# Kernel tuning notes

Hardware: AMD Instinct MI355X
Metric: run time of the kernel (lower is better)

Reference implementation:

```python
import jax, jax.numpy as jnp
import numpy as np

B, N, DIM = 4, 4096, 512
HEADS, DHEAD, CHUNK = 4, 128, 64
MAX_LR = 1.0
EPS = 1e-6


def rmsnorm(x):
    return x * jax.lax.rsqrt(jnp.mean(x * x, axis=-1, keepdims=True) + EPS)


def mem_mlp(params, x):
    # MemoryMLP depth=2: x @ W1 -> silu -> @ W2 (no biases)
    W1, W2 = params
    return jax.nn.silu(x @ W1) @ W2


def assoc_scan(gates, x):
    # linear recurrence y_i = g_i * y_{i-1} + x_i along axis=1 (chunks)
    def op(a, b):
        ga, xa = a
        gb, xb = b
        return (ga * gb, gb * xa + xb)
    _, y = jax.lax.associative_scan(op, (gates, x), axis=1)
    return y


def setup_inputs() -> dict:
    key = jax.random.key(0)
    ks = jax.random.split(key, 12)
    di = HEADS * DHEAD
    nrm = lambda k, shp, sc: jax.random.normal(k, shp, jnp.float32) * sc
    return {
        'seq': nrm(ks[0], (B, N, DIM), 1.0),
        'g_store': jnp.ones((DIM,), jnp.float32),
        'g_retrieve': jnp.ones((DIM,), jnp.float32),
        'W_q': nrm(ks[1], (DIM, di), DIM ** -0.5),
        'W_kv': nrm(ks[2], (DIM, 2 * di), DIM ** -0.5),
        'W_step': nrm(ks[3], (DIM, HEADS), DIM ** -0.5),
        'W_mom': nrm(ks[4], (DIM, HEADS), DIM ** -0.5),
        'W_decay': nrm(ks[5], (DIM, HEADS), DIM ** -0.5),
        'W_gate': nrm(ks[6], (DIM, HEADS), DIM ** -0.5),
        'gamma_mh': jnp.zeros((HEADS, 1, DHEAD), jnp.float32),
        'W_o': nrm(ks[7], (di, DIM), di ** -0.5),
        'M_W1': nrm(ks[8], (DHEAD, DHEAD), DHEAD ** -0.5),
        'M_W2': nrm(ks[9], (DHEAD, DHEAD), DHEAD ** -0.5),
    }


def reference(seq, g_store, g_retrieve, W_q, W_kv, W_step, W_mom, W_decay,
              W_gate, gamma_mh, W_o, M_W1, M_W2):
    b, n, dim = seq.shape
    h, d, c = HEADS, DHEAD, CHUNK
    nc = n // c
    bh = b * h

    # ---------------- store path ----------------
    s = rmsnorm(seq) * g_store                                   # (b,n,dim)
    lr = jax.nn.sigmoid(s @ W_step) * MAX_LR                     # (b,n,h)
    lr_c = lr.transpose(0, 2, 1).reshape(bh, nc, c)              # (bh,nc,c)
    chunked = s.reshape(b, nc, c, dim).mean(2)                   # (b,nc,dim)
    decay = jax.nn.sigmoid(chunked @ W_decay).transpose(0, 2, 1).reshape(bh, nc)
    mom = jax.nn.sigmoid(chunked @ W_mom).transpose(0, 2, 1).reshape(bh, nc)

    kv = s @ W_kv                                                # (b,n,2*h*d)
    k, v = jnp.split(kv, 2, axis=-1)
    to_chunks = lambda t: t.reshape(b, n, h, d).transpose(0, 2, 1, 3).reshape(bh, nc, c, d)
    k, v = to_chunks(k), to_chunks(v)

    # per-chunk gradient at the initial memory weights (vmap(grad))
    def chunk_loss(params, kc, lrc, vc):
        pred = mem_mlp(params, kc)                               # (c,d)
        loss = jnp.mean((pred - vc) ** 2, axis=-1)               # (c,)
        return jnp.sum(loss * lrc)

    gfn = jax.vmap(jax.vmap(jax.grad(chunk_loss),
                            in_axes=((None, None), 0, 0, 0)),
                   in_axes=((None, None), 0, 0, 0))
    g1, g2 = gfn((M_W1, M_W2), k, lr_c, v)                       # (bh,nc,d,d)
    s1, s2 = -g1, -g2                                            # surprises

    # momentum assoc scan: m_i = mom_i * m_{i-1} + s_i
    momg = mom[:, :, None, None]
    m1 = assoc_scan(momg, s1)
    m2 = assoc_scan(momg, s2)

    # decay-gated weight recurrence with prev = initial weights:
    # W_i = (1 - decay_i) * W_{i-1} + m_i,  W_0 = init
    def scan_with_init(gates, x, w0):
        g = jnp.concatenate([jnp.ones_like(gates[:, :1]), gates], axis=1)
        x0 = jnp.broadcast_to(w0, (bh, 1) + w0.shape)
        return assoc_scan(g, jnp.concatenate([x0, x], axis=1))   # (bh,nc+1,d,d)

    dg = (1.0 - decay)[:, :, None, None]
    u1 = scan_with_init(dg, m1, M_W1)
    u2 = scan_with_init(dg, m2, M_W2)
    # retrieval for chunk i uses weights after chunk i-1 (paper semantics)
    w1c, w2c = u1[:, :-1], u2[:, :-1]                            # (bh,nc,d,d)

    # ---------------- retrieve path ----------------
    r = rmsnorm(seq) * g_retrieve
    q = to_chunks(r @ W_q)                                       # (bh,nc,c,d)
    pred = jax.vmap(jax.vmap(lambda w1, w2, qc: mem_mlp((w1, w2), qc)))(w1c, w2c, q)
    out = pred.reshape(b, h, n, d)
    out = rmsnorm(out) * (gamma_mh + 1.0)                        # multihead rmsnorm
    gate = jax.nn.sigmoid(r @ W_gate)                            # (b,n,h)
    out = out * gate.transpose(0, 2, 1)[..., None]               # retrieve gate
    out = out.transpose(0, 2, 1, 3).reshape(b, n, h * d)         # merge heads
    return out @ W_o                                             # combine heads
```

## Files before the change

### kernel.cpp

```cpp
#include <hip/hip_runtime.h>

typedef unsigned short u16;
typedef unsigned int u32;
typedef __attribute__((ext_vector_type(8))) short s16x8;
typedef __attribute__((ext_vector_type(4))) float f32x4;

#define DEV __device__ __forceinline__
#define MFMA16(a,b,c) __builtin_amdgcn_mfma_f32_16x16x32_bf16(a,b,c,0,0,0)

DEV float bf2f(u16 x){ u32 u=((u32)x)<<16; float f; __builtin_memcpy(&f,&u,4); return f; }
DEV u16 f2bf(float f){ u32 u; __builtin_memcpy(&u,&f,4); u32 r=u+0x7FFFu+((u>>16)&1u); return (u16)(r>>16); }
DEV uint4 pack8(const float* f){
  uint4 v;
  v.x=(u32)f2bf(f[0])|((u32)f2bf(f[1])<<16);
  v.y=(u32)f2bf(f[2])|((u32)f2bf(f[3])<<16);
  v.z=(u32)f2bf(f[4])|((u32)f2bf(f[5])<<16);
  v.w=(u32)f2bf(f[6])|((u32)f2bf(f[7])<<16);
  return v;
}
DEV float sigm(float x){ return 1.0f/(1.0f+__expf(-x)); }


DEV void trans_tile_a(const float* src, u16* dst, int K, int Nn, int bx, int by,
                      int tid, bool act, float* ld)
{
  int n0 = bx*64, k0 = by*64;
  if (act){
    #pragma unroll
    for (int rr=0; rr<4; rr++){
      int kk = rr*16 + (tid>>4);
      int nn = (tid&15)*4;
      float4 v = *(const float4*)(src + (size_t)(k0+kk)*Nn + n0 + nn);
      ld[kk*65+nn]=v.x; ld[kk*65+nn+1]=v.y; ld[kk*65+nn+2]=v.z; ld[kk*65+nn+3]=v.w;
    }
  }
  __syncthreads();
  if (act){
    int nn2 = tid>>2, kb = (tid&3)*16;
    float o[16];
    #pragma unroll
    for (int j=0;j<16;j++) o[j] = ld[(kb+j)*65+nn2];
    u16* dp = dst + (size_t)(n0+nn2)*K + k0 + kb;
    *(uint4*)dp     = pack8(&o[0]);
    *(uint4*)(dp+8) = pack8(&o[8]);
  }
}

__global__ __launch_bounds__(512) void k_front(const float* __restrict__ seq,
    const float* __restrict__ gs, const float* __restrict__ gr,
    const float* __restrict__ Wstep, const float* __restrict__ Wgate,
    const float* __restrict__ Wdec, const float* __restrict__ Wmom,
    const float* __restrict__ Wkv, const float* __restrict__ Wq,
    const float* __restrict__ Wo, const float* __restrict__ MW1,
    const float* __restrict__ MW2,
    u16* __restrict__ s, u16* __restrict__ r,
    float* __restrict__ lr, float* __restrict__ gate,
    float* __restrict__ momv, float* __restrict__ dgv,
    u16* __restrict__ Wkvt, u16* __restrict__ Wqt, u16* __restrict__ Wot,
    u16* __restrict__ W1t, u16* __restrict__ W2t, u16* __restrict__ W2s)
{
  __shared__ float smem[8192];
  const int blk = blockIdx.x;
  const int tid = threadIdx.x;

  if (blk >= 256){
    int l = blk - 256;
    bool act = tid < 256;
    int t2 = tid & 255;
    if (l < 128)      trans_tile_a(Wkv, Wkvt, 512, 1024, l&15, l>>4, t2, act, smem);
    else if (l < 192){ int m = l-128; trans_tile_a(Wq, Wqt, 512, 512, m&7, m>>3, t2, act, smem); }
    else if (l < 256){ int m = l-192; trans_tile_a(Wo, Wot, 512, 512, m&7, m>>3, t2, act, smem); }
    else if (l < 260){ int m = l-256; trans_tile_a(MW1, W1t, 128, 128, m&1, m>>1, t2, act, smem); }
    else if (l < 264){ int m = l-260; trans_tile_a(MW2, W2t, 128, 128, m&1, m>>1, t2, act, smem); }
    else {
      __syncthreads();
      if (act){
        int e = ((l-264)*256 + t2)*8;
        float f[8];
        *(float4*)&f[0] = *(const float4*)(MW2+e);
        *(float4*)&f[4] = *(const float4*)(MW2+e+4);
        *(uint4*)(W2s+e) = pack8(f);
      }
    }
    return;
  }

  float* pchunk = smem;
  float* red    = smem + 4096;
  const int b = blk >> 6, ci = blk & 63;
  const int wv = tid >> 6, lane = tid & 63;
  const size_t rowbase = (size_t)b*4096 + (size_t)ci*64;

  float psum[8] = {0,0,0,0,0,0,0,0};
  #pragma unroll 1
  for (int tt=0; tt<8; tt++){
    int t = wv*8 + tt;
    const float* row = seq + (rowbase + t)*512;
    float x[8];
    *(float4*)&x[0] = *(const float4*)(row + lane*8);
    *(float4*)&x[4] = *(const float4*)(row + lane*8 + 4);
    float ss = 0.f;
    #pragma unroll
    for (int j=0;j<8;j++) ss += x[j]*x[j];
    #pragma unroll
    for (int o=32;o>=1;o>>=1) ss += __shfl_xor(ss, o, 64);
    float inv = rsqrtf(ss*(1.0f/512.0f) + 1e-6f);
    float al[4] = {0,0,0,0}, ag[4] = {0,0,0,0};
    float sv8[8], rv8[8];
    #pragma unroll
    for (int j=0;j<8;j++){
      int d = lane*8 + j;
      float sn = x[j]*inv;
      float sv = sn*gs[d];
      float rv = sn*gr[d];
      sv8[j]=sv; rv8[j]=rv;
      psum[j] += sv;
      float4 wst = *(const float4*)(Wstep + d*4);
      float4 wgt = *(const float4*)(Wgate + d*4);
      al[0]+=sv*wst.x; al[1]+=sv*wst.y; al[2]+=sv*wst.z; al[3]+=sv*wst.w;
      ag[0]+=rv*wgt.x; ag[1]+=rv*wgt.y; ag[2]+=rv*wgt.z; ag[3]+=rv*wgt.w;
    }
    *(uint4*)(s + (rowbase+t)*512 + lane*8) = pack8(sv8);
    *(uint4*)(r + (rowbase+t)*512 + lane*8) = pack8(rv8);
    #pragma unroll
    for (int o=32;o>=1;o>>=1){
      #pragma unroll
      for (int h=0;h<4;h++){ al[h] += __shfl_xor(al[h], o, 64); ag[h] += __shfl_xor(ag[h], o, 64); }
    }
    if (lane == 0){
      #pragma unroll
      for (int h=0;h<4;h++){
        lr[(rowbase+t)*4 + h]   = sigm(al[h]);
        gate[(rowbase+t)*4 + h] = sigm(ag[h]);
      }
    }
  }
  #pragma unroll
  for (int j=0;j<8;j++) pchunk[wv*512 + lane*8+j] = psum[j];
  __syncthreads();
  {
    int d = tid;
    float mean = 0.f;
    #pragma unroll
    for (int w=0;w<8;w++) mean += pchunk[w*512 + d];
    mean *= (1.0f/64.0f);
    #pragma unroll
    for (int h=0;h<4;h++){
      red[h*512 + d]     = mean*Wdec[d*4+h];
      red[(4+h)*512 + d] = mean*Wmom[d*4+h];
    }
  }
  __syncthreads();
  {
    float sum = 0.f;
    #pragma unroll
    for (int j=0;j<8;j++) sum += red[wv*512 + lane*8+j];
    #pragma unroll
    for (int o=32;o>=1;o>>=1) sum += __shfl_xor(sum, o, 64);
    if (lane == 0){
      if (wv < 4) dgv[((size_t)(b*4+wv))*64 + ci]      = 1.0f - sigm(sum);
      else        momv[((size_t)(b*4+(wv-4)))*64 + ci] = sigm(sum);
    }
  }
}

template<bool OUT_BF>
DEV void gemm_body(const u16* A, const u16* Bt, void* Cv, int K, int ldc,
                   int bx, int by, u16* sA, u16* sB)
{
  const int tid = threadIdx.x;
  const int wv = tid>>6, lane = tid&63, lrow = lane&15, lk = lane>>4;
  const int wm = (wv>>1)*64, wn = (wv&1)*64;
  const int rowbase = by*128, colbase = bx*128;
  const int srow = lane>>3;
  const int scol = (lane&7)*8;
  f32x4 acc[4][4] = {};
  for (int kc = 0; kc < K; kc += 64){
    __syncthreads();
    #pragma unroll
    for (int it=0; it<4; ++it){
      int seg = it*4 + wv;
      int row = seg*8 + srow;
      __builtin_amdgcn_global_load_lds(
        (const __attribute__((address_space(1))) void*)(A + (size_t)(rowbase+row)*K + kc + scol),
        (__attribute__((address_space(3))) void*)&sA[seg*512 + lane*8], 16, 0, 0);
      __builtin_amdgcn_global_load_lds(
        (const __attribute__((address_space(1))) void*)(Bt + (size_t)(colbase+row)*K + kc + scol),
        (__attribute__((address_space(3))) void*)&sB[seg*512 + lane*8], 16, 0, 0);
    }
    __syncthreads();
    #pragma unroll
    for (int k0=0;k0<2;k0++){
      s16x8 a[4], b[4];
      #pragma unroll
      for (int m=0;m<4;m++) a[m] = *(const s16x8*)&sA[(wm+m*16+lrow)*64 + k0*32 + lk*8];
      #pragma unroll
      for (int n=0;n<4;n++) b[n] = *(const s16x8*)&sB[(wn+n*16+lrow)*64 + k0*32 + lk*8];
      #pragma unroll
      for (int m=0;m<4;m++)
        #pragma unroll
        for (int n=0;n<4;n++)
          acc[m][n] = MFMA16(a[m], b[n], acc[m][n]);
    }
  }
  #pragma unroll
  for (int m=0;m<4;m++)
    #pragma unroll
    for (int n=0;n<4;n++)
      #pragma unroll
      for (int r=0;r<4;r++){
        int row = rowbase + wm + m*16 + lk*4 + r;
        int col = colbase + wn + n*16 + lrow;
        float v = acc[m][n][r];
        if (OUT_BF) ((u16*)Cv)[(size_t)row*ldc + col] = f2bf(v);
        else        ((float*)Cv)[(size_t)row*ldc + col] = v;
      }
}

__global__ __launch_bounds__(256) void k_gemmAB(const u16* __restrict__ A1,
    const u16* __restrict__ B1, u16* __restrict__ C1,
    const u16* __restrict__ A2, const u16* __restrict__ B2, u16* __restrict__ C2)
{
  __shared__ u16 sA[128*64];
  __shared__ u16 sB[128*64];
  int bid = blockIdx.x;
  if (bid < 1024){
    int s = (bid & 7)*128 + (bid >> 3);
    gemm_body<true>(A1, B1, C1, 512, 1024, s & 7, s >> 3, sA, sB);
  } else {
    int l = bid - 1024;
    int s = (l & 7)*64 + (l >> 3);
    gemm_body<true>(A2, B2, C2, 512, 512, s & 3, s >> 2, sA, sB);
  }
}

template<bool OUT_BF>
__global__ __launch_bounds__(256) void k_gemm1(const u16* __restrict__ A,
    const u16* __restrict__ Bt, void* __restrict__ Cv, int K, int ldc, int nbx, int cpx)
{
  __shared__ u16 sA[128*64];
  __shared__ u16 sB[128*64];
  int bid = blockIdx.x;
  int s = (bid & 7)*cpx + (bid >> 3);
  gemm_body<OUT_BF>(A, Bt, Cv, K, ldc, s % nbx, s / nbx, sA, sB);
}

__global__ __launch_bounds__(256,4) void k_grad(const u16* __restrict__ kv,
    const float* __restrict__ lr, const u16* __restrict__ W1t,
    const u16* __restrict__ W2t, const u16* __restrict__ W2s,
    u16* __restrict__ s1, u16* __restrict__ s2)
{
  __shared__ u16 bufR[64*136];
  __shared__ u16 bufAt[128*68];
  __shared__ u16 bufPt[128*68];
  __shared__ float lrs[64];

  const int blk = blockIdx.x;
  const int bhi = blk >> 6, ci = blk & 63;
  const int b = bhi >> 2, hd = bhi & 3;
  const int tid = threadIdx.x;
  const int wv = tid>>6, lane = tid&63, lrow = lane&15, lk = lane>>4;
  int col[2]; col[0] = wv*32 + lrow; col[1] = wv*32 + 16 + lrow;
  const int f_hi[2] = { (lrow>>3)*128, ((16+lrow)>>3)*128 };
  const int f_lo[2] = { lrow&7, (16+lrow)&7 };
  const int fbase = wv*512;
  const size_t rowbase = (size_t)b*4096 + (size_t)ci*64;
  const u16* kvb = kv + rowbase*1024 + hd*128;

  #pragma unroll
  for (int rep=0;rep<4;rep++){
    int lin = rep*2048 + tid*8;
    int i = lin >> 7, d = lin & 127;
    *(uint4*)&bufR[i*136 + d]  = *(const uint4*)(kvb + (size_t)i*1024 + d);
    *(uint4*)&bufPt[i*136 + d] = *(const uint4*)(kvb + (size_t)i*1024 + 512 + d);
  }
  if (tid < 64) lrs[tid] = lr[(rowbase + tid)*4 + hd] * (2.0f/128.0f);
  __syncthreads();

  float spv[4][2][4];

  {
    f32x4 acc[4][2] = {};
    #pragma unroll
    for (int k0=0;k0<4;k0++){
      s16x8 w0 = *(const s16x8*)(W1t + col[0]*128 + k0*32 + lk*8);
      s16x8 w1 = *(const s16x8*)(W1t + col[1]*128 + k0*32 + lk*8);
      #pragma unroll
      for (int m=0;m<4;m++){
        s16x8 a = *(const s16x8*)&bufR[(m*16+lrow)*136 + k0*32 + lk*8];
        acc[m][0] = MFMA16(a, w0, acc[m][0]);
        acc[m][1] = MFMA16(a, w1, acc[m][1]);
      }
    }
    __syncthreads();
    #pragma unroll
    for (int m=0;m<4;m++)
      #pragma unroll
      for (int n=0;n<2;n++){
        int row0 = m*16 + lk*4;
        u16 av4[4];
        #pragma unroll
        for (int r=0;r<4;r++){
          float h = acc[m][n][r];
          float sg = sigm(h);
          av4[r] = f2bf(h*sg);
          spv[m][n][r] = sg*(1.0f + h*(1.0f - sg));
          bufR[(row0+r)*136 + col[n]] = av4[r];
        }
        *(uint2*)&bufAt[col[n]*68 + row0] = make_uint2(
          (u32)av4[0] | ((u32)av4[1]<<16), (u32)av4[2] | ((u32)av4[3]<<16));
      }
  }
  __syncthreads();

  {
    f32x4 acc[4][2] = {};
    #pragma unroll
    for (int k0=0;k0<4;k0++){
      s16x8 w0 = *(const s16x8*)(W2t + col[0]*128 + k0*32 + lk*8);
      s16x8 w1 = *(const s16x8*)(W2t + col[1]*128 + k0*32 + lk*8);
      #pragma unroll
      for (int m=0;m<4;m++){
        s16x8 a = *(const s16x8*)&bufR[(m*16+lrow)*136 + k0*32 + lk*8];
        acc[m][0] = MFMA16(a, w0, acc[m][0]);
        acc[m][1] = MFMA16(a, w1, acc[m][1]);
      }
    }
    u16 vv[4][2][4];
    #pragma unroll
    for (int m=0;m<4;m++)
      #pragma unroll
      for (int n=0;n<2;n++)
        #pragma unroll
        for (int r=0;r<4;r++)
          vv[m][n][r] = bufPt[(m*16+lk*4+r)*136 + col[n]];
    __syncthreads();
    #pragma unroll
    for (int m=0;m<4;m++)
      #pragma unroll
      for (int n=0;n<2;n++){
        int row0 = m*16 + lk*4;
        u16 dp4[4];
        #pragma unroll
        for (int r=0;r<4;r++){
          float dp = lrs[row0+r]*(acc[m][n][r] - bf2f(vv[m][n][r]));
          dp4[r] = f2bf(dp);
          bufR[(row0+r)*136 + col[n]] = dp4[r];
        }
        *(uint2*)&bufPt[col[n]*68 + row0] = make_uint2(
          (u32)dp4[0] | ((u32)dp4[1]<<16), (u32)dp4[2] | ((u32)dp4[3]<<16));
      }
  }
  __syncthreads();

  {
    f32x4 da[4][2] = {};
    #pragma unroll
    for (int k0=0;k0<4;k0++){
      s16x8 w0 = *(const s16x8*)(W2s + col[0]*128 + k0*32 + lk*8);
      s16x8 w1 = *(const s16x8*)(W2s + col[1]*128 + k0*32 + lk*8);
      #pragma unroll
      for (int m=0;m<4;m++){
        s16x8 a = *(const s16x8*)&bufR[(m*16+lrow)*136 + k0*32 + lk*8];
        da[m][0] = MFMA16(a, w0, da[m][0]);
        da[m][1] = MFMA16(a, w1, da[m][1]);
      }
    }
    __syncthreads();
    #pragma unroll
    for (int m=0;m<4;m++)
      #pragma unroll
      for (int n=0;n<2;n++){
        int row0 = m*16 + lk*4;
        u16 dh4[4];
        #pragma unroll
        for (int r=0;r<4;r++) dh4[r] = f2bf(spv[m][n][r]*da[m][n][r]);
        *(uint2*)&bufR[col[n]*68 + row0] = make_uint2(
          (u32)dh4[0] | ((u32)dh4[1]<<16), (u32)dh4[2] | ((u32)dh4[3]<<16));
      }
  }

  const size_t outbase = (size_t)blk * 16384;

  s16x8 kbf[2][2];
  #pragma unroll
  for (int n=0;n<2;n++)
    #pragma unroll
    for (int k0=0;k0<2;k0++)
      #pragma unroll
      for (int j=0;j<8;j++)
        ((u16*)&kbf[n][k0])[j] = kvb[(size_t)(k0*32 + lk*8 + j)*1024 + col[n]];
  {
    f32x4 acc[8][2] = {};
    #pragma unroll
    for (int k0=0;k0<2;k0++){
      s16x8 bf0 = *(const s16x8*)&bufAt[col[0]*68 + k0*32 + lk*8];
      s16x8 bf1 = *(const s16x8*)&bufAt[col[1]*68 + k0*32 + lk*8];
      #pragma unroll
      for (int m=0;m<8;m++){
        s16x8 a = *(const s16x8*)&bufPt[(m*16+lrow)*68 + k0*32 + lk*8];
        acc[m][0] = MFMA16(a, bf0, acc[m][0]);
        acc[m][1] = MFMA16(a, bf1, acc[m][1]);
      }
    }
    #pragma unroll
    for (int m=0;m<8;m++)
      #pragma unroll
      for (int n=0;n<2;n++)
        #pragma unroll
        for (int r=0;r<4;r++)
          s2[outbase + m*2048 + fbase + f_hi[n] + (lk*4+r)*8 + f_lo[n]] = f2bf(-acc[m][n][r]);
  }
  __syncthreads();

  {
    f32x4 acc[8][2] = {};
    #pragma unroll
    for (int k0=0;k0<2;k0++)
      #pragma unroll
      for (int m=0;m<8;m++){
        s16x8 a = *(const s16x8*)&bufR[(m*16+lrow)*68 + k0*32 + lk*8];
        acc[m][0] = MFMA16(a, kbf[0][k0], acc[m][0]);
        acc[m][1] = MFMA16(a, kbf[1][k0], acc[m][1]);
      }
    #pragma unroll
    for (int m=0;m<8;m++)
      #pragma unroll
      for (int n=0;n<2;n++)
        #pragma unroll
        for (int r=0;r<4;r++)
          s1[outbase + m*2048 + fbase + f_hi[n] + (lk*4+r)*8 + f_lo[n]] = f2bf(-acc[m][n][r]);
  }
}

__global__ __launch_bounds__(256) void k_scan(const float* __restrict__ momv,
    const float* __restrict__ dgv, const float* __restrict__ MW1,
    const float* __restrict__ MW2, u16* __restrict__ s1w, u16* __restrict__ s2w)
{
  int bhi = blockIdx.x >> 4, eb = blockIdx.x & 15;
  int e0 = eb*1024 + threadIdx.x*4;
  int colD = ((e0>>11)<<4) + ((e0>>3)&15);
  int kD   = ((e0>>9)&3)*32 + ((e0>>7)&3)*8 + (e0&7);
  float u1[4], u2[4], m1[4]={0,0,0,0}, m2[4]={0,0,0,0};
  #pragma unroll
  for (int j=0;j<4;j++){
    u1[j] = MW1[(kD+j)*128 + colD];
    u2[j] = MW2[(kD+j)*128 + colD];
  }
  size_t base = (size_t)bhi*64*16384 + e0;
  const float* mv = momv + bhi*64;
  const float* dv = dgv + bhi*64;
  #pragma unroll 4
  for (int t=0; t<64; t++){
    float g  = mv[t];
    float dg = dv[t];
    size_t idx = base + (size_t)t*16384;
    uint2 a = *(const uint2*)(s1w + idx);
    uint2 c = *(const uint2*)(s2w + idx);
    uint2 w1o, w2o;
    w1o.x = (u32)f2bf(u1[0]) | ((u32)f2bf(u1[1])<<16);
    w1o.y = (u32)f2bf(u1[2]) | ((u32)f2bf(u1[3])<<16);
    w2o.x = (u32)f2bf(u2[0]) | ((u32)f2bf(u2[1])<<16);
    w2o.y = (u32)f2bf(u2[2]) | ((u32)f2bf(u2[3])<<16);
    *(uint2*)(s1w + idx) = w1o;
    *(uint2*)(s2w + idx) = w2o;
    u16 ah[4] = {(u16)(a.x&0xffffu),(u16)(a.x>>16),(u16)(a.y&0xffffu),(u16)(a.y>>16)};
    u16 ch[4] = {(u16)(c.x&0xffffu),(u16)(c.x>>16),(u16)(c.y&0xffffu),(u16)(c.y>>16)};
    #pragma unroll
    for (int j=0;j<4;j++){
      m1[j] = g*m1[j] + bf2f(ah[j]);
      m2[j] = g*m2[j] + bf2f(ch[j]);
      u1[j] = dg*u1[j] + m1[j];
      u2[j] = dg*u2[j] + m2[j];
    }
  }
}

__global__ __launch_bounds__(512) void k_retr(const u16* __restrict__ qin,
    const u16* __restrict__ w1c, const u16* __restrict__ w2c,
    const float* __restrict__ gate, const float* __restrict__ gamma,
    u16* __restrict__ outp)
{
  __shared__ u16 bufQ[64*136];
  __shared__ u16 bufA[64*132];
  __shared__ float rsum[8][64];
  const int blk = blockIdx.x;
  const int bhi = blk >> 6, ci = blk & 63;
  const int b = bhi >> 2, hd = bhi & 3;
  const int tid = threadIdx.x;
  const int wv = tid>>6, lane = tid&63, lrow = lane&15, lk = lane>>4;
  const int colw = wv*16 + lrow;
  const size_t rowbase = (size_t)b*4096 + (size_t)ci*64;
  const u16* w1 = w1c + (size_t)blk*16384;
  const u16* w2 = w2c + (size_t)blk*16384;
  const int lane8 = lane*8;

  #pragma unroll
  for (int rep=0;rep<2;rep++){
    int lin = rep*4096 + tid*8;
    int i = lin>>7, d = lin&127;
    *(uint4*)&bufQ[i*136 + d] = *(const uint4*)(qin + (rowbase+i)*512 + hd*128 + d);
  }
  __syncthreads();

  {
    s16x8 wf[4];
    #pragma unroll
    for (int k0=0;k0<4;k0++) wf[k0] = *(const s16x8*)(w1 + wv*2048 + k0*512 + lane8);
    f32x4 acc[4] = {};
    #pragma unroll
    for (int k0=0;k0<4;k0++){
      #pragma unroll
      for (int m=0;m<4;m++){
        s16x8 a = *(const s16x8*)&bufQ[(m*16+lrow)*136 + k0*32 + lk*8];
        acc[m] = MFMA16(a, wf[k0], acc[m]);
      }
    }
    #pragma unroll
    for (int m=0;m<4;m++){
      #pragma unroll
      for (int r=0;r<4;r++){
        float h = acc[m][r];
        bufA[(m*16+lk*4+r)*132 + colw] = f2bf(h*sigm(h));
      }
    }
  }
  __syncthreads();

  f32x4 acc[4] = {};
  {
    s16x8 wf[4];
    #pragma unroll
    for (int k0=0;k0<4;k0++) wf[k0] = *(const s16x8*)(w2 + wv*2048 + k0*512 + lane8);
    #pragma unroll
    for (int k0=0;k0<4;k0++){
      #pragma unroll
      for (int m=0;m<4;m++){
        s16x8 a = *(const s16x8*)&bufA[(m*16+lrow)*132 + k0*32 + lk*8];
        acc[m] = MFMA16(a, wf[k0], acc[m]);
      }
    }
  }
  #pragma unroll
  for (int m=0;m<4;m++){
    #pragma unroll
    for (int r=0;r<4;r++){
      float p = acc[m][r]*acc[m][r];
      p += __shfl_xor(p, 1, 64);
      p += __shfl_xor(p, 2, 64);
      p += __shfl_xor(p, 4, 64);
      p += __shfl_xor(p, 8, 64);
      if (lrow == 0) rsum[wv][m*16 + lk*4 + r] = p;
    }
  }
  __syncthreads();
  float gm = gamma[hd*128 + colw] + 1.0f;
  #pragma unroll
  for (int m=0;m<4;m++){
    #pragma unroll
    for (int r=0;r<4;r++){
      int row = m*16 + lk*4 + r;
      float sum = rsum[0][row]+rsum[1][row]+rsum[2][row]+rsum[3][row]
                + rsum[4][row]+rsum[5][row]+rsum[6][row]+rsum[7][row];
      float inv = rsqrtf(sum*(1.0f/128.0f) + 1e-6f);
      float gt = gate[(rowbase+row)*4 + hd];
      outp[(rowbase+row)*512 + hd*128 + colw] = f2bf(acc[m][r]*inv*gm*gt);
    }
  }
}

extern "C" void kernel_launch(void* const* d_in, const int* in_sizes, int n_in,
                              void* d_out, int out_size, void* d_ws, size_t ws_size,
                              hipStream_t stream)
{
  const float* seq    = (const float*)d_in[0];
  const float* gstore = (const float*)d_in[1];
  const float* gret   = (const float*)d_in[2];
  const float* W_q    = (const float*)d_in[3];
  const float* W_kv   = (const float*)d_in[4];
  const float* W_step = (const float*)d_in[5];
  const float* W_mom  = (const float*)d_in[6];
  const float* W_dec  = (const float*)d_in[7];
  const float* W_gate = (const float*)d_in[8];
  const float* gamma  = (const float*)d_in[9];
  const float* W_o    = (const float*)d_in[10];
  const float* MW1    = (const float*)d_in[11];
  const float* MW2    = (const float*)d_in[12];
  float* out = (float*)d_out;

  const size_t NS = (size_t)16384*512;
  const size_t NG = (size_t)16*64*16384;
  size_t need = (5*NS + 2*NG + 524288 + 262144 + 262144 + 3*16384)*2
              + (2*65536 + 2048)*4;
  if (ws_size < need) return;

  char* ws = (char*)d_ws;
  u16* s_bf = (u16*)ws; ws += NS*2;
  u16* r_bf = (u16*)ws; ws += NS*2;
  u16* kv_bf= (u16*)ws; ws += 2*NS*2;
  u16* q_bf = (u16*)ws; ws += NS*2;
  u16* s1   = (u16*)ws; ws += NG*2;
  u16* s2   = (u16*)ws; ws += NG*2;
  u16* Wkvt = (u16*)ws; ws += (size_t)524288*2;
  u16* Wqt  = (u16*)ws; ws += (size_t)262144*2;
  u16* Wot  = (u16*)ws; ws += (size_t)262144*2;
  u16* W1tb = (u16*)ws; ws += (size_t)16384*2;
  u16* W2tb = (u16*)ws; ws += (size_t)16384*2;
  u16* W2sb = (u16*)ws; ws += (size_t)16384*2;
  float* lr   = (float*)ws; ws += (size_t)65536*4;
  float* gatep= (float*)ws; ws += (size_t)65536*4;
  float* momv = (float*)ws; ws += 1024*4;
  float* dgv  = (float*)ws; ws += 1024*4;
  u16* outp = s_bf;

  k_front<<<528, 512, 0, stream>>>(seq, gstore, gret, W_step, W_gate, W_dec, W_mom,
                                   W_kv, W_q, W_o, MW1, MW2,
                                   s_bf, r_bf, lr, gatep, momv, dgv,
                                   Wkvt, Wqt, Wot, W1tb, W2tb, W2sb);
  k_gemmAB<<<1536, 256, 0, stream>>>(s_bf, Wkvt, kv_bf, r_bf, Wqt, q_bf);
  k_grad<<<1024, 256, 0, stream>>>(kv_bf, lr, W1tb, W2tb, W2sb, s1, s2);
  k_scan<<<256, 256, 0, stream>>>(momv, dgv, MW1, MW2, s1, s2);
  k_retr<<<1024, 512, 0, stream>>>(q_bf, s1, s2, gatep, gamma, outp);
  k_gemm1<false><<<512, 256, 0, stream>>>(outp, Wot, out, 512, 512, 4, 64);
}
```

Baseline: 169.8 us.

## Process two chunks per k_grad block and prefetch the next chunk's kv during the last GEMM

Each k_grad block now handles two consecutive chunks instead of one, halving the grid to 512 blocks. Shared buffers are rotated across the two passes. The second chunk's k/v tile and learning rates are loaded into the freed buffers while the final dW1 outer-product GEMM of the first chunk runs, to overlap global loads with MFMA work. The trade-off is fewer blocks for occupancy and latency hiding, plus more complex buffer aliasing that must keep the barriers correct.

```diff
diff --git a/kernel.cpp b/kernel.cpp
--- a/kernel.cpp
+++ b/kernel.cpp
@@ -250,13 +250,13 @@
     const u16* __restrict__ W2t, const u16* __restrict__ W2s,
     u16* __restrict__ s1, u16* __restrict__ s2)
 {
-  __shared__ u16 bufR[64*136];
-  __shared__ u16 bufAt[128*68];
-  __shared__ u16 bufPt[128*68];
+  __shared__ u16 bufA[64*136];
+  __shared__ u16 bufB[64*136];
+  __shared__ u16 bufC[64*136];
   __shared__ float lrs[64];
 
   const int blk = blockIdx.x;
-  const int bhi = blk >> 6, ci = blk & 63;
+  const int bhi = blk >> 5, cih = blk & 31;
   const int b = bhi >> 2, hd = bhi & 3;
   const int tid = threadIdx.x;
   const int wv = tid>>6, lane = tid&63, lrow = lane&15, lk = lane>>4;
@@ -264,172 +264,196 @@
   const int f_hi[2] = { (lrow>>3)*128, ((16+lrow)>>3)*128 };
   const int f_lo[2] = { lrow&7, (16+lrow)&7 };
   const int fbase = wv*512;
-  const size_t rowbase = (size_t)b*4096 + (size_t)ci*64;
-  const u16* kvb = kv + rowbase*1024 + hd*128;
-
-  #pragma unroll
-  for (int rep=0;rep<4;rep++){
-    int lin = rep*2048 + tid*8;
-    int i = lin >> 7, d = lin & 127;
-    *(uint4*)&bufR[i*136 + d]  = *(const uint4*)(kvb + (size_t)i*1024 + d);
-    *(uint4*)&bufPt[i*136 + d] = *(const uint4*)(kvb + (size_t)i*1024 + 512 + d);
-  }
-  if (tid < 64) lrs[tid] = lr[(rowbase + tid)*4 + hd] * (2.0f/128.0f);
-  __syncthreads();
-
-  float spv[4][2][4];
 
   {
-    f32x4 acc[4][2] = {};
-    #pragma unroll
-    for (int k0=0;k0<4;k0++){
-      s16x8 w0 = *(const s16x8*)(W1t + col[0]*128 + k0*32 + lk*8);
-      s16x8 w1 = *(const s16x8*)(W1t + col[1]*128 + k0*32 + lk*8);
-      #pragma unroll
-      for (int m=0;m<4;m++){
-        s16x8 a = *(const s16x8*)&bufR[(m*16+lrow)*136 + k0*32 + lk*8];
-        acc[m][0] = MFMA16(a, w0, acc[m][0]);
-        acc[m][1] = MFMA16(a, w1, acc[m][1]);
-      }
-    }
+    const size_t rowbase0 = (size_t)b*4096 + (size_t)(cih*2)*64;
+    const u16* kvb0 = kv + rowbase0*1024 + hd*128;
+    #pragma unroll 2
+    for (int rep=0;rep<4;rep++){
+      int lin = rep*2048 + tid*8;
+      int i = lin >> 7, d = lin & 127;
+      *(uint4*)&bufA[i*136 + d] = *(const uint4*)(kvb0 + (size_t)i*1024 + d);
+      *(uint4*)&bufC[i*136 + d] = *(const uint4*)(kvb0 + (size_t)i*1024 + 512 + d);
+    }
+    if (tid < 64) lrs[tid] = lr[(rowbase0 + tid)*4 + hd] * (2.0f/128.0f);
+  }
+
+  #pragma unroll 1
+  for (int p=0; p<2; p++){
+    u16* R = p ? bufB : bufA;
+    u16* T = p ? bufA : bufB;
+    u16* V = bufC;
+    const int chunk = cih*2 + p;
+    const size_t rowbase = (size_t)b*4096 + (size_t)chunk*64;
+    const u16* kvb = kv + rowbase*1024 + hd*128;
+    const size_t outbase = (size_t)(bhi*64 + chunk) * 16384;
+
     __syncthreads();
-    #pragma unroll
-    for (int m=0;m<4;m++)
-      #pragma unroll
-      for (int n=0;n<2;n++){
-        int row0 = m*16 + lk*4;
-        u16 av4[4];
-        #pragma unroll
-        for (int r=0;r<4;r++){
-          float h = acc[m][n][r];
-          float sg = sigm(h);
-          av4[r] = f2bf(h*sg);
-          spv[m][n][r] = sg*(1.0f + h*(1.0f - sg));
-          bufR[(row0+r)*136 + col[n]] = av4[r];
-        }
-        *(uint2*)&bufAt[col[n]*68 + row0] = make_uint2(
-          (u32)av4[0] | ((u32)av4[1]<<16), (u32)av4[2] | ((u32)av4[3]<<16));
-      }
-  }
-  __syncthreads();
-
-  {
-    f32x4 acc[4][2] = {};
-    #pragma unroll
-    for (int k0=0;k0<4;k0++){
-      s16x8 w0 = *(const s16x8*)(W2t + col[0]*128 + k0*32 + lk*8);
-      s16x8 w1 = *(const s16x8*)(W2t + col[1]*128 + k0*32 + lk*8);
-      #pragma unroll
-      for (int m=0;m<4;m++){
-        s16x8 a = *(const s16x8*)&bufR[(m*16+lrow)*136 + k0*32 + lk*8];
-        acc[m][0] = MFMA16(a, w0, acc[m][0]);
-        acc[m][1] = MFMA16(a, w1, acc[m][1]);
-      }
-    }
-    u16 vv[4][2][4];
-    #pragma unroll
-    for (int m=0;m<4;m++)
-      #pragma unroll
-      for (int n=0;n<2;n++)
-        #pragma unroll
-        for (int r=0;r<4;r++)
-          vv[m][n][r] = bufPt[(m*16+lk*4+r)*136 + col[n]];
+
+    float spv[4][2][4];
+
+    {
+      f32x4 acc[4][2] = {};
+      #pragma unroll
+      for (int k0=0;k0<4;k0++){
+        s16x8 w0 = *(const s16x8*)(W1t + col[0]*128 + k0*32 + lk*8);
+        s16x8 w1 = *(const s16x8*)(W1t + col[1]*128 + k0*32 + lk*8);
+        #pragma unroll
+        for (int m=0;m<4;m++){
+          s16x8 a = *(const s16x8*)&R[(m*16+lrow)*136 + k0*32 + lk*8];
+          acc[m][0] = MFMA16(a, w0, acc[m][0]);
+          acc[m][1] = MFMA16(a, w1, acc[m][1]);
+        }
+      }
+      __syncthreads();
+      #pragma unroll
+      for (int m=0;m<4;m++)
+        #pragma unroll
+        for (int n=0;n<2;n++){
+          int row0 = m*16 + lk*4;
+          u16 av4[4];
+          #pragma unroll
+          for (int r=0;r<4;r++){
+            float h = acc[m][n][r];
+            float sg = sigm(h);
+            av4[r] = f2bf(h*sg);
+            spv[m][n][r] = sg*(1.0f + h*(1.0f - sg));
+            R[(row0+r)*136 + col[n]] = av4[r];
+          }
+          *(uint2*)&T[col[n]*68 + row0] = make_uint2(
+            (u32)av4[0] | ((u32)av4[1]<<16), (u32)av4[2] | ((u32)av4[3]<<16));
+        }
+    }
     __syncthreads();
-    #pragma unroll
-    for (int m=0;m<4;m++)
-      #pragma unroll
-      for (int n=0;n<2;n++){
-        int row0 = m*16 + lk*4;
-        u16 dp4[4];
-        #pragma unroll
-        for (int r=0;r<4;r++){
-          float dp = lrs[row0+r]*(acc[m][n][r] - bf2f(vv[m][n][r]));
-          dp4[r] = f2bf(dp);
-          bufR[(row0+r)*136 + col[n]] = dp4[r];
-        }
-        *(uint2*)&bufPt[col[n]*68 + row0] = make_uint2(
-          (u32)dp4[0] | ((u32)dp4[1]<<16), (u32)dp4[2] | ((u32)dp4[3]<<16));
-      }
-  }
-  __syncthreads();
-
-  {
-    f32x4 da[4][2] = {};
-    #pragma unroll
-    for (int k0=0;k0<4;k0++){
-      s16x8 w0 = *(const s16x8*)(W2s + col[0]*128 + k0*32 + lk*8);
-      s16x8 w1 = *(const s16x8*)(W2s + col[1]*128 + k0*32 + lk*8);
-      #pragma unroll
-      for (int m=0;m<4;m++){
-        s16x8 a = *(const s16x8*)&bufR[(m*16+lrow)*136 + k0*32 + lk*8];
-        da[m][0] = MFMA16(a, w0, da[m][0]);
-        da[m][1] = MFMA16(a, w1, da[m][1]);
-      }
+
+    {
+      f32x4 acc[4][2] = {};
+      #pragma unroll
+      for (int k0=0;k0<4;k0++){
+        s16x8 w0 = *(const s16x8*)(W2t + col[0]*128 + k0*32 + lk*8);
+        s16x8 w1 = *(const s16x8*)(W2t + col[1]*128 + k0*32 + lk*8);
+        #pragma unroll
+        for (int m=0;m<4;m++){
+          s16x8 a = *(const s16x8*)&R[(m*16+lrow)*136 + k0*32 + lk*8];
+          acc[m][0] = MFMA16(a, w0, acc[m][0]);
+          acc[m][1] = MFMA16(a, w1, acc[m][1]);
+        }
+      }
+      u16 vv[4][2][4];
+      #pragma unroll
+      for (int m=0;m<4;m++)
+        #pragma unroll
+        for (int n=0;n<2;n++)
+          #pragma unroll
+          for (int r=0;r<4;r++)
+            vv[m][n][r] = V[(m*16+lk*4+r)*136 + col[n]];
+      __syncthreads();
+      #pragma unroll
+      for (int m=0;m<4;m++)
+        #pragma unroll
+        for (int n=0;n<2;n++){
+          int row0 = m*16 + lk*4;
+          u16 dp4[4];
+          #pragma unroll
+          for (int r=0;r<4;r++){
+            float dp = lrs[row0+r]*(acc[m][n][r] - bf2f(vv[m][n][r]));
+            dp4[r] = f2bf(dp);
+            R[(row0+r)*136 + col[n]] = dp4[r];
+          }
+          *(uint2*)&V[col[n]*68 + row0] = make_uint2(
+            (u32)dp4[0] | ((u32)dp4[1]<<16), (u32)dp4[2] | ((u32)dp4[3]<<16));
+        }
     }
     __syncthreads();
-    #pragma unroll
-    for (int m=0;m<4;m++)
-      #pragma unroll
-      for (int n=0;n<2;n++){
-        int row0 = m*16 + lk*4;
-        u16 dh4[4];
-        #pragma unroll
-        for (int r=0;r<4;r++) dh4[r] = f2bf(spv[m][n][r]*da[m][n][r]);
-        *(uint2*)&bufR[col[n]*68 + row0] = make_uint2(
-          (u32)dh4[0] | ((u32)dh4[1]<<16), (u32)dh4[2] | ((u32)dh4[3]<<16));
-      }
-  }
-
-  const size_t outbase = (size_t)blk * 16384;
-
-  s16x8 kbf[2][2];
-  #pragma unroll
-  for (int n=0;n<2;n++)
-    #pragma unroll
-    for (int k0=0;k0<2;k0++)
-      #pragma unroll
-      for (int j=0;j<8;j++)
-        ((u16*)&kbf[n][k0])[j] = kvb[(size_t)(k0*32 + lk*8 + j)*1024 + col[n]];
-  {
-    f32x4 acc[8][2] = {};
-    #pragma unroll
-    for (int k0=0;k0<2;k0++){
-      s16x8 bf0 = *(const s16x8*)&bufAt[col[0]*68 + k0*32 + lk*8];
-      s16x8 bf1 = *(const s16x8*)&bufAt[col[1]*68 + k0*32 + lk*8];
-      #pragma unroll
-      for (int m=0;m<8;m++){
-        s16x8 a = *(const s16x8*)&bufPt[(m*16+lrow)*68 + k0*32 + lk*8];
-        acc[m][0] = MFMA16(a, bf0, acc[m][0]);
-        acc[m][1] = MFMA16(a, bf1, acc[m][1]);
-      }
-    }
-    #pragma unroll
-    for (int m=0;m<8;m++)
-      #pragma unroll
-      for (int n=0;n<2;n++)
-        #pragma unroll
-        for (int r=0;r<4;r++)
-          s2[outbase + m*2048 + fbase + f_hi[n] + (lk*4+r)*8 + f_lo[n]] = f2bf(-acc[m][n][r]);
-  }
-  __syncthreads();
-
-  {
-    f32x4 acc[8][2] = {};
-    #pragma unroll
-    for (int k0=0;k0<2;k0++)
-      #pragma unroll
-      for (int m=0;m<8;m++){
-        s16x8 a = *(const s16x8*)&bufR[(m*16+lrow)*68 + k0*32 + lk*8];
-        acc[m][0] = MFMA16(a, kbf[0][k0], acc[m][0]);
-        acc[m][1] = MFMA16(a, kbf[1][k0], acc[m][1]);
-      }
-    #pragma unroll
-    for (int m=0;m<8;m++)
-      #pragma unroll
-      for (int n=0;n<2;n++)
-        #pragma unroll
-        for (int r=0;r<4;r++)
-          s1[outbase + m*2048 + fbase + f_hi[n] + (lk*4+r)*8 + f_lo[n]] = f2bf(-acc[m][n][r]);
+
+    {
+      f32x4 da[4][2] = {};
+      #pragma unroll
+      for (int k0=0;k0<4;k0++){
+        s16x8 w0 = *(const s16x8*)(W2s + col[0]*128 + k0*32 + lk*8);
+        s16x8 w1 = *(const s16x8*)(W2s + col[1]*128 + k0*32 + lk*8);
+        #pragma unroll
+        for (int m=0;m<4;m++){
+          s16x8 a = *(const s16x8*)&R[(m*16+lrow)*136 + k0*32 + lk*8];
+          da[m][0] = MFMA16(a, w0, da[m][0]);
+          da[m][1] = MFMA16(a, w1, da[m][1]);
+        }
+      }
+      __syncthreads();
+      #pragma unroll
+      for (int m=0;m<4;m++)
+        #pragma unroll
+        for (int n=0;n<2;n++){
+          int row0 = m*16 + lk*4;
+          u16 dh4[4];
+          #pragma unroll
+          for (int r=0;r<4;r++) dh4[r] = f2bf(spv[m][n][r]*da[m][n][r]);
+          *(uint2*)&R[col[n]*68 + row0] = make_uint2(
+            (u32)dh4[0] | ((u32)dh4[1]<<16), (u32)dh4[2] | ((u32)dh4[3]<<16));
+        }
+    }
+
+    s16x8 kbf[2][2];
+    #pragma unroll
+    for (int n=0;n<2;n++)
+      #pragma unroll
+      for (int k0=0;k0<2;k0++)
+        #pragma unroll
+        for (int j=0;j<8;j++)
+          ((u16*)&kbf[n][k0])[j] = kvb[(size_t)(k0*32 + lk*8 + j)*1024 + col[n]];
+    {
+      f32x4 acc[8][2] = {};
+      #pragma unroll
+      for (int k0=0;k0<2;k0++){
+        s16x8 bf0 = *(const s16x8*)&T[col[0]*68 + k0*32 + lk*8];
+        s16x8 bf1 = *(const s16x8*)&T[col[1]*68 + k0*32 + lk*8];
+        #pragma unroll
+        for (int m=0;m<8;m++){
+          s16x8 a = *(const s16x8*)&V[(m*16+lrow)*68 + k0*32 + lk*8];
+          acc[m][0] = MFMA16(a, bf0, acc[m][0]);
+          acc[m][1] = MFMA16(a, bf1, acc[m][1]);
+        }
+      }
+      #pragma unroll
+      for (int m=0;m<8;m++)
+        #pragma unroll
+        for (int n=0;n<2;n++)
+          #pragma unroll
+          for (int r=0;r<4;r++)
+            s2[outbase + m*2048 + fbase + f_hi[n] + (lk*4+r)*8 + f_lo[n]] = f2bf(-acc[m][n][r]);
+    }
+    __syncthreads();
+
+    if (p == 0){
+      const u16* kvb2 = kvb + (size_t)64*1024;
+      #pragma unroll 2
+      for (int rep=0;rep<4;rep++){
+        int lin = rep*2048 + tid*8;
+        int i = lin >> 7, d = lin & 127;
+        *(uint4*)&T[i*136 + d] = *(const uint4*)(kvb2 + (size_t)i*1024 + d);
+        *(uint4*)&V[i*136 + d] = *(const uint4*)(kvb2 + (size_t)i*1024 + 512 + d);
+      }
+      if (tid < 64) lrs[tid] = lr[(rowbase + 64 + tid)*4 + hd] * (2.0f/128.0f);
+    }
+
+    {
+      f32x4 acc[8][2] = {};
+      #pragma unroll
+      for (int k0=0;k0<2;k0++)
+        #pragma unroll
+        for (int m=0;m<8;m++){
+          s16x8 a = *(const s16x8*)&R[(m*16+lrow)*68 + k0*32 + lk*8];
+          acc[m][0] = MFMA16(a, kbf[0][k0], acc[m][0]);
+          acc[m][1] = MFMA16(a, kbf[1][k0], acc[m][1]);
+        }
+      #pragma unroll
+      for (int m=0;m<8;m++)
+        #pragma unroll
+        for (int n=0;n<2;n++)
+          #pragma unroll
+          for (int r=0;r<4;r++)
+            s1[outbase + m*2048 + fbase + f_hi[n] + (lk*4+r)*8 + f_lo[n]] = f2bf(-acc[m][n][r]);
+    }
   }
 }
 
@@ -618,7 +642,7 @@
                                    s_bf, r_bf, lr, gatep, momv, dgv,
                                    Wkvt, Wqt, Wot, W1tb, W2tb, W2sb);
   k_gemmAB<<<1536, 256, 0, stream>>>(s_bf, Wkvt, kv_bf, r_bf, Wqt, q_bf);
-  k_grad<<<1024, 256, 0, stream>>>(kv_bf, lr, W1tb, W2tb, W2sb, s1, s2);
+  k_grad<<<512, 256, 0, stream>>>(kv_bf, lr, W1tb, W2tb, W2sb, s1, s2);
   k_scan<<<256, 256, 0, stream>>>(momv, dgv, MW1, MW2, s1, s2);
   k_retr<<<1024, 512, 0, stream>>>(q_bf, s1, s2, gatep, gamma, outp);
   k_gemm1<false><<<512, 256, 0, stream>>>(outp, Wot, out, 512, 512, 4, 64);
```

Measured after the change: 184.7 us. +8.8%, slower.
